# Performance work log

Measured on AMD Instinct MI355X. Metric: run time of the kernel, lower is better.

Reference implementation:

```python
import jax, jax.numpy as jnp
import numpy as np

W_CTX = 4   # sliding window half-width (self.w)
TOP = 6     # querysim top-k
KMAX = 2    # k-max pooling per n-gram


def setup_inputs() -> dict:
    key = jax.random.key(0)
    ks = jax.random.split(key, 16)
    n_words, E = 50000, 300
    B, Q, D = 128, 16, 800
    emb = jax.random.normal(ks[0], (n_words, E), jnp.float32)
    emb = emb / jnp.linalg.norm(emb, axis=1, keepdims=True)
    emb_table = jnp.concatenate([emb, jnp.zeros((1, E), jnp.float32)], 0)  # padding row
    return {
        'qrls_words': jax.random.randint(ks[1], (B, Q), 0, n_words),
        'doc_words': jax.random.randint(ks[2], (B, D), 0, n_words),
        'emb_table': emb_table,
        'idf_table': jax.random.uniform(ks[3], (n_words + 1,), jnp.float32),
        'conv1_w': jax.random.normal(ks[4], (32, 1, 1, 1), jnp.float32) * 0.1,
        'conv1_b': jnp.zeros((32,), jnp.float32),
        'conv2_w': jax.random.normal(ks[5], (32, 1, 2, 2), jnp.float32) * 0.1,
        'conv2_b': jnp.zeros((32,), jnp.float32),
        'conv3_w': jax.random.normal(ks[6], (32, 1, 3, 3), jnp.float32) * 0.1,
        'conv3_b': jnp.zeros((32,), jnp.float32),
        'w1': jax.random.normal(ks[7], (13 * Q, 32), jnp.float32) * 0.05,
        'b1': jnp.zeros((32,), jnp.float32),
        'w2': jax.random.normal(ks[8], (32, 32), jnp.float32) * 0.1,
        'b2': jnp.zeros((32,), jnp.float32),
        'w3': jax.random.normal(ks[9], (32, 1), jnp.float32) * 0.1,
        'b3': jnp.zeros((1,), jnp.float32),
    }


def _cosine_simmat(a, b):
    # a: [B,A,E], b: [B,T,E] -> [B,A,T]; denominators each get +1e-9 (as in torch code)
    an = jnp.linalg.norm(a, axis=2)[:, :, None] + 1e-9
    bn = jnp.linalg.norm(b, axis=2)[:, None, :] + 1e-9
    return jnp.einsum('bae,bte->bat', a, b) / (an * bn)


def _context(demb):
    # sliding-window sum over [max(0,i-w), min(L,i+w)) then /(2w+1)
    B, L, E = demb.shape
    csum = jnp.concatenate([jnp.zeros((B, 1, E), demb.dtype), jnp.cumsum(demb, axis=1)], axis=1)
    i = jnp.arange(L)
    s = jnp.maximum(0, i - W_CTX)
    e = jnp.minimum(L, i + W_CTX)
    return (csum[:, e] - csum[:, s]) / (2 * W_CTX + 1)


def _pacrr_conv(simmat, w, b, ng):
    # simmat: [B,1,Q,D]; pad right/bottom by ng-1, valid conv -> same Q,D
    conv = jax.lax.conv_general_dilated(
        simmat, w, (1, 1), [(0, ng - 1), (0, ng - 1)],
        dimension_numbers=('NCHW', 'OIHW', 'NCHW')) + b[None, :, None, None]
    conv = jax.nn.relu(conv)
    top_f = conv.max(axis=1)                      # max over filters: [B,Q,D]
    return jax.lax.top_k(top_f, KMAX)[0]          # k-max over doc dim: [B,Q,KMAX]


def reference(qrls_words, doc_words, emb_table, idf_table,
              conv1_w, conv1_b, conv2_w, conv2_b, conv3_w, conv3_b,
              w1, b1, w2, b2, w3, b3):
    idf = idf_table[qrls_words][..., None]                 # [B,Q,1]
    qemb = emb_table[qrls_words]                           # [B,Q,E]
    demb = emb_table[doc_words]                            # [B,D,E]
    context = _context(demb)
    querysim = jax.lax.top_k(_cosine_simmat(qemb, context), TOP)[0]  # [B,Q,TOP]
    simmat = _cosine_simmat(qemb, demb)[:, None]           # [B,1,Q,D]
    scores = jnp.concatenate([
        _pacrr_conv(simmat, conv1_w, conv1_b, 1),
        _pacrr_conv(simmat, conv2_w, conv2_b, 2),
        _pacrr_conv(simmat, conv3_w, conv3_b, 3),
    ], axis=2)                                             # [B,Q,3*KMAX]
    scores = jnp.concatenate([scores, querysim, idf], axis=-1)  # [B,Q,13]
    x = scores.reshape(scores.shape[0], -1)
    x = jax.nn.relu(x @ w1 + b1)
    x = jax.nn.relu(x @ w2 + b2)
    return x @ w3 + b3                                     # [B,1]
```

## Files before the change

### kernel.cpp

```cpp
#include <hip/hip_runtime.h>
#include <float.h>
#include <math.h>

#define NB 128
#define NQ 16
#define ND 800
#define NE 300
#define ZROW 50000

#define WS_SIM    0
#define WS_CTXINV (NB*NQ*ND)
#define WS_SCORES (WS_CTXINV + NB*ND)
#define WS_C2     (WS_SCORES + NB*NQ*13)
#define WS_QBF    (WS_C2 + NB*NQ*3*26)

#define HP 164

typedef __attribute__((ext_vector_type(8))) short short8;
typedef __attribute__((ext_vector_type(4))) float f32x4;
typedef __attribute__((ext_vector_type(4))) unsigned short ushort4v;

__device__ __forceinline__ unsigned short f2bf(float x) {
    unsigned u = __float_as_uint(x);
    u += 0x7FFF + ((u >> 16) & 1);
    return (unsigned short)(u >> 16);
}

__device__ __forceinline__ void ins6(float t[6], float v) {
    if (v > t[5]) t[5] = v;
    float a;
    if (t[5] > t[4]) { a = t[4]; t[4] = t[5]; t[5] = a; }
    if (t[4] > t[3]) { a = t[3]; t[3] = t[4]; t[4] = a; }
    if (t[3] > t[2]) { a = t[2]; t[2] = t[3]; t[3] = a; }
    if (t[2] > t[1]) { a = t[1]; t[1] = t[2]; t[2] = a; }
    if (t[1] > t[0]) { a = t[0]; t[0] = t[1]; t[1] = a; }
}

__device__ __forceinline__ void ins2(float& a1, float& a2, float v) {
    if (v > a2) a2 = v;
    if (a2 > a1) { float t = a1; a1 = a2; a2 = t; }
}

__device__ __forceinline__ void merge2(float& a1, float& a2, float b1v, float b2v) {
    float hi = fmaxf(a1, b1v), lo = fminf(a1, b1v);
    a1 = hi;
    a2 = fmaxf(lo, fmaxf(a2, b2v));
}

__global__ __launch_bounds__(256) void kq(const int* __restrict__ qrls,
                                          const float* __restrict__ emb,
                                          const float* __restrict__ idf,
                                          float* __restrict__ ws) {
    int b = blockIdx.x;
    int tid = threadIdx.x;
    __shared__ int qrow[16];
    if (tid < 16) qrow[tid] = qrls[b * NQ + tid];
    __syncthreads();
    unsigned short* qbf = (unsigned short*)(ws + WS_QBF) + (size_t)b * 16 * 320;
    for (int it = tid; it < 1200; it += 256) {
        int q = it / 75, e4 = it - q * 75;
        float4 v = *(const float4*)(emb + (size_t)qrow[q] * NE + e4 * 4);
        ushort4v u;
        u[0] = f2bf(v.x); u[1] = f2bf(v.y); u[2] = f2bf(v.z); u[3] = f2bf(v.w);
        *(ushort4v*)(qbf + q * 320 + e4 * 4) = u;
    }
    if (tid < 160) {
        int q = tid / 10, p = tid - q * 10;
        *(unsigned*)(qbf + q * 320 + 300 + p * 2) = 0u;
    }
    if (tid < NQ)
        ws[WS_SCORES + (b * NQ + tid) * 13 + 12] = idf[qrow[tid]];
}

__global__ __launch_bounds__(256, 5) void kfused(const int* __restrict__ docw,
                                                 const float* __restrict__ emb,
                                                 float* __restrict__ ws) {
    int b = blockIdx.y;
    int base = blockIdx.x * 32;
    int tid = threadIdx.x;
    __shared__ float slds[6656];
    __shared__ int sidx[40];
    __shared__ float ACC[32][33];

    int wv = tid >> 6, lane = tid & 63;

    if (tid < 40) {
        int rg = base - 4 + tid;
        sidx[tid] = (rg >= 0 && rg < ND) ? docw[b * ND + rg] : ZROW;
    }
    for (int i = tid; i < 32 * 33; i += 256) ((float*)ACC)[i] = 0.f;
    __syncthreads();

    int rsub = lane & 15, kgrp = lane >> 4;
    const unsigned short* qp = (const unsigned short*)(ws + WS_QBF)
                               + ((size_t)b * 16 + rsub) * 320 + kgrp * 8;
    int lrb = (4 + wv * 16 + rsub) * HP + kgrp * 8;
    int w0 = (wv == 3) ? 16 : 0;

    f32x4 acc = {0.f, 0.f, 0.f, 0.f};

#pragma unroll
    for (int h = 0; h < 2; ++h) {
        for (int j = wv; j < 26; j += 4) {
            int jj = __builtin_amdgcn_readfirstlane(j);
            int F = jj * 64 + lane;
            int r = F / 41;
            int c4 = F - r * 41;
            int g4 = h * 40 + c4;
            bool ok = (r < 40) && (c4 < 40) && (g4 < 75);
            int rowsrc = ok ? sidx[r] : ZROW;
            int colsrc = ok ? g4 * 4 : 0;
            const float* gp = emb + (size_t)rowsrc * NE + colsrc;
            __builtin_amdgcn_global_load_lds(
                (const __attribute__((address_space(1))) void*)gp,
                (__attribute__((address_space(3))) void*)&slds[(size_t)jj * 256],
                16, 0, 0);
        }
        __syncthreads();

        if (wv < 2) {
#pragma unroll
            for (int k = 0; k < 5; ++k) {
                int c0 = k * 32;
                float4 x0 = *(const float4*)&slds[lrb + c0];
                float4 x1 = *(const float4*)&slds[lrb + c0 + 4];
                short8 bf;
                bf[0] = (short)f2bf(x0.x); bf[1] = (short)f2bf(x0.y);
                bf[2] = (short)f2bf(x0.z); bf[3] = (short)f2bf(x0.w);
                bf[4] = (short)f2bf(x1.x); bf[5] = (short)f2bf(x1.y);
                bf[6] = (short)f2bf(x1.z); bf[7] = (short)f2bf(x1.w);
                short8 af = *(const short8*)(qp + h * 160 + c0);
                acc = __builtin_amdgcn_mfma_f32_16x16x32_bf16(af, bf, acc, 0, 0, 0);
            }
        } else {
            float cw0 = 0.f, cw1 = 0.f, cw2 = 0.f;
            for (int i = 0; i < 23; ++i) {
                int r = w0 + i;
                float2 va = *(const float2*)&slds[r * HP + 2 * lane];
                float vc = (lane < 32) ? slds[r * HP + 128 + lane] : 0.f;
                cw0 += va.x; cw1 += va.y; cw2 += vc;
                if (i >= 8) {
                    int r2 = r - 8;
                    float2 vb = *(const float2*)&slds[r2 * HP + 2 * lane];
                    float vd = (lane < 32) ? slds[r2 * HP + 128 + lane] : 0.f;
                    cw0 -= vb.x; cw1 -= vb.y; cw2 -= vd;
                }
                if (i >= 7) {
                    float s = fmaf(cw0, cw0, fmaf(cw1, cw1, cw2 * cw2));
                    s += __shfl_xor(s, 1);
                    if ((lane & 1) == 0)
                        ACC[r - 7][lane >> 1] += s;
                }
            }
        }
        __syncthreads();
    }

    if (wv < 2) {
        int col = base + wv * 16 + rsub;
        float* simp = ws + WS_SIM + (size_t)b * NQ * ND + col;
#pragma unroll
        for (int i = 0; i < 4; ++i)
            simp[(size_t)(kgrp * 4 + i) * ND] = acc[i];
    } else if (wv == 2 && lane < 32) {
        float s = 0.f;
#pragma unroll
        for (int j = 0; j < 32; ++j) s += ACC[lane][j];
        ws[WS_CTXINV + b * ND + base + lane] =
            1.f / (sqrtf(s) * (1.f / 9.f) + 1e-9f);
    }
}

__global__ __launch_bounds__(256) void ktail2(const float* __restrict__ c1w,
                                              const float* __restrict__ c1b,
                                              const float* __restrict__ c2w,
                                              const float* __restrict__ c2b,
                                              const float* __restrict__ c3w,
                                              const float* __restrict__ c3b,
                                              float* __restrict__ ws) {
    int b = blockIdx.y;
    int bx = blockIdx.x;
    int tid = threadIdx.x;
    __shared__ float BUF[3216];
    __shared__ float PART[4][16][6];
    __shared__ float WL[160 * 4];
    int wv = tid >> 6, lane = tid & 63;

    if (bx < 13) {
        if (tid < 160) {
            int f = tid / 5, j = tid - f * 5;
            float4 w;
            if (j == 0)      w = make_float4(c3w[9*f],   c3w[9*f+1], c3w[9*f+2], c3w[9*f+3]);
            else if (j == 1) w = make_float4(c3w[9*f+4], c3w[9*f+5], c3w[9*f+6], c3w[9*f+7]);
            else if (j == 2) w = make_float4(c3w[9*f+8], c3b[f],     c1w[f],     c1b[f]);
            else if (j == 3) w = make_float4(c2w[4*f],   c2w[4*f+1], c2w[4*f+2], c2w[4*f+3]);
            else             w = make_float4(c2b[f],     0.f,        0.f,        0.f);
            *(float4*)&WL[tid * 4] = w;
        }
        int c0 = bx * 64;
        for (int idx = tid; idx < 18 * 66; idx += 256) {
            int r = idx / 66, c = idx % 66;
            int d = c0 + c;
            float v = 0.f;
            if (r < NQ && d < ND) v = ws[WS_SIM + (size_t)(b * NQ + r) * ND + d];
            BUF[r * 68 + c] = v;
        }
        __syncthreads();

        int q = tid & 15, dg = tid >> 4;
        int cb = dg * 4;
        float s0[6], s1[6], s2[6];
#pragma unroll
        for (int i = 0; i < 6; ++i) {
            s0[i] = BUF[q * 68 + cb + i];
            s1[i] = BUF[(q + 1) * 68 + cb + i];
            s2[i] = BUF[(q + 2) * 68 + cb + i];
        }
        float m1[4], m2[4], m3[4];
#pragma unroll
        for (int i = 0; i < 4; ++i) { m1[i] = -FLT_MAX; m2[i] = -FLT_MAX; m3[i] = -FLT_MAX; }
        const float4* WL4 = (const float4*)WL;
        for (int f = 0; f < 32; ++f) {
            float4 wA = WL4[f * 5];
            float4 wB = WL4[f * 5 + 1];
            float4 wC = WL4[f * 5 + 2];
            float4 wD = WL4[f * 5 + 3];
            float4 wE = WL4[f * 5 + 4];
#pragma unroll
            for (int i = 0; i < 4; ++i) {
                float v1 = fmaf(wC.z, s0[i], wC.w);
                m1[i] = fmaxf(m1[i], v1);
                float v2 = wE.x;
                v2 = fmaf(wD.x, s0[i], v2); v2 = fmaf(wD.y, s0[i+1], v2);
                v2 = fmaf(wD.z, s1[i], v2); v2 = fmaf(wD.w, s1[i+1], v2);
                m2[i] = fmaxf(m2[i], v2);
                float v3 = wC.y;
                v3 = fmaf(wA.x, s0[i], v3); v3 = fmaf(wA.y, s0[i+1], v3); v3 = fmaf(wA.z, s0[i+2], v3);
                v3 = fmaf(wA.w, s1[i], v3); v3 = fmaf(wB.x, s1[i+1], v3); v3 = fmaf(wB.y, s1[i+2], v3);
                v3 = fmaf(wB.z, s2[i], v3); v3 = fmaf(wB.w, s2[i+1], v3); v3 = fmaf(wC.x, s2[i+2], v3);
                m3[i] = fmaxf(m3[i], v3);
            }
        }
        float a1[3] = {-FLT_MAX, -FLT_MAX, -FLT_MAX};
        float a2[3] = {-FLT_MAX, -FLT_MAX, -FLT_MAX};
#pragma unroll
        for (int i = 0; i < 4; ++i) {
            if (c0 + cb + i < ND) {
                ins2(a1[0], a2[0], fmaxf(m1[i], 0.f));
                ins2(a1[1], a2[1], fmaxf(m2[i], 0.f));
                ins2(a1[2], a2[2], fmaxf(m3[i], 0.f));
            }
        }
#pragma unroll
        for (int m = 16; m <= 32; m <<= 1) {
#pragma unroll
            for (int ng = 0; ng < 3; ++ng) {
                float b1v = __shfl_xor(a1[ng], m), b2v = __shfl_xor(a2[ng], m);
                merge2(a1[ng], a2[ng], b1v, b2v);
            }
        }
        if (lane < 16) {
#pragma unroll
            for (int ng = 0; ng < 3; ++ng) {
                PART[wv][lane][ng * 2]     = a1[ng];
                PART[wv][lane][ng * 2 + 1] = a2[ng];
            }
        }
        __syncthreads();
        if (tid < 16) {
            float* c2p = ws + WS_C2 + ((size_t)(b * NQ + tid) * 3) * 26 + bx * 2;
#pragma unroll
            for (int ng = 0; ng < 3; ++ng) {
                float x1 = PART[0][tid][ng * 2], x2 = PART[0][tid][ng * 2 + 1];
#pragma unroll
                for (int p = 1; p < 4; ++p)
                    merge2(x1, x2, PART[p][tid][ng * 2], PART[p][tid][ng * 2 + 1]);
                c2p[ng * 26] = x1; c2p[ng * 26 + 1] = x2;
            }
        }
    } else {
        int q = (bx - 13) * 4 + wv;
        float* P = &BUF[wv * 804];
        const float* simrow = ws + WS_SIM + (size_t)(b * NQ + q) * ND;
        const float* cinv = ws + WS_CTXINV + (size_t)b * ND;
        float carry = 0.f;
        for (int c = 0; c < 13; ++c) {
            int d = c * 64 + lane;
            float v = (d < ND) ? simrow[d] : 0.f;
#pragma unroll
            for (int off = 1; off < 64; off <<= 1) {
                float t = __shfl_up(v, off);
                if (lane >= off) v += t;
            }
            v += carry;
            if (d < ND) P[d] = v;
            carry = __shfl(v, 63);
        }
        float top[6] = {-FLT_MAX,-FLT_MAX,-FLT_MAX,-FLT_MAX,-FLT_MAX,-FLT_MAX};
        for (int c = 0; c < 13; ++c) {
            int d = c * 64 + lane;
            if (d < ND) {
                int hi_i = (d + 3 < ND) ? d + 3 : ND - 1;
                float hi = P[hi_i];
                float lo = (d >= 5) ? P[d - 5] : 0.f;
                float ctx = (hi - lo) * (1.f / 9.f) * cinv[d];
                ins6(top, ctx);
            }
        }
#pragma unroll
        for (int m = 1; m < 64; m <<= 1) {
            float o0 = __shfl_xor(top[0], m), o1 = __shfl_xor(top[1], m);
            float o2 = __shfl_xor(top[2], m), o3 = __shfl_xor(top[3], m);
            float o4 = __shfl_xor(top[4], m), o5 = __shfl_xor(top[5], m);
            ins6(top, o0); ins6(top, o1); ins6(top, o2);
            ins6(top, o3); ins6(top, o4); ins6(top, o5);
        }
        if (lane == 0) {
            float* sc = ws + WS_SCORES + (size_t)(b * NQ + q) * 13;
            sc[6] = top[0]; sc[7] = top[1]; sc[8]  = top[2];
            sc[9] = top[3]; sc[10] = top[4]; sc[11] = top[5];
        }
    }
}

__global__ __launch_bounds__(64) void kmlp(const float* __restrict__ w1,
                                           const float* __restrict__ b1,
                                           const float* __restrict__ w2,
                                           const float* __restrict__ b2,
                                           const float* __restrict__ w3,
                                           const float* __restrict__ b3,
                                           const float* __restrict__ ws,
                                           float* __restrict__ out) {
    int b = blockIdx.x, tid = threadIdx.x;
    __shared__ float sc[208];
    const float* s = ws + WS_SCORES + (size_t)b * 208;
    for (int i = tid; i < 208; i += 64)
        if ((i % 13) >= 6) sc[i] = s[i];
    if (tid < 48) {
        int q = tid / 3, ng = tid % 3;
        const float* p = ws + WS_C2 + ((size_t)(b * NQ + q) * 3 + ng) * 26;
        float x1 = p[0], x2 = p[1];
#pragma unroll
        for (int st = 1; st < 13; ++st) merge2(x1, x2, p[st * 2], p[st * 2 + 1]);
        sc[q * 13 + ng * 2] = x1; sc[q * 13 + ng * 2 + 1] = x2;
    }
    __syncthreads();
    int j = tid & 31, half = tid >> 5;
    float a = 0.f;
    int i0 = half * 104;
    for (int i = 0; i < 104; ++i) a = fmaf(sc[i0 + i], w1[(i0 + i) * 32 + j], a);
    a += __shfl_xor(a, 32);
    a = fmaxf(a + b1[j], 0.f);
    float a2v = 0.f;
    for (int k = 0; k < 32; ++k) {
        float hk = __shfl(a, k);
        a2v = fmaf(hk, w2[k * 32 + j], a2v);
    }
    a2v = fmaxf(a2v + b2[j], 0.f);
    float r = a2v * w3[j];
    if (half) r = 0.f;
#pragma unroll
    for (int m = 1; m <= 32; m <<= 1) r += __shfl_xor(r, m);
    if (tid == 0) out[b] = r + b3[0];
}

extern "C" void kernel_launch(void* const* d_in, const int* in_sizes, int n_in,
                              void* d_out, int out_size, void* d_ws, size_t ws_size,
                              hipStream_t stream) {
    (void)in_sizes; (void)n_in; (void)out_size; (void)ws_size;
    const int*   qrls = (const int*)d_in[0];
    const int*   docw = (const int*)d_in[1];
    const float* emb  = (const float*)d_in[2];
    const float* idf  = (const float*)d_in[3];
    const float* c1w  = (const float*)d_in[4];
    const float* c1b  = (const float*)d_in[5];
    const float* c2w  = (const float*)d_in[6];
    const float* c2b  = (const float*)d_in[7];
    const float* c3w  = (const float*)d_in[8];
    const float* c3b  = (const float*)d_in[9];
    const float* w1   = (const float*)d_in[10];
    const float* b1   = (const float*)d_in[11];
    const float* w2   = (const float*)d_in[12];
    const float* b2   = (const float*)d_in[13];
    const float* w3   = (const float*)d_in[14];
    const float* b3   = (const float*)d_in[15];
    float* ws  = (float*)d_ws;
    float* out = (float*)d_out;

    kq<<<dim3(NB), 256, 0, stream>>>(qrls, emb, idf, ws);
    kfused<<<dim3(25, NB), 256, 0, stream>>>(docw, emb, ws);
    ktail2<<<dim3(17, NB), 256, 0, stream>>>(c1w, c1b, c2w, c2b, c3w, c3b, ws);
    kmlp<<<dim3(NB), 64, 0, stream>>>(w1, b1, w2, b2, w3, b3, ws, out);
}
```

Before: 84.09 us.

## Double-buffer embedding staging in five column chunks to overlap loads with MFMA

The fused sim/context kernel used to stage each 160-column half of the document embeddings into LDS, then wait before computing. It now stages 64-column chunks into two alternating LDS buffers, issuing the next chunk's async global-to-LDS loads while the current chunk feeds the MFMA and sliding-window norm work. The smaller LDS footprint allows launch bounds to be raised from 5 to 6 blocks per CU, and float-to-bf16 conversion now uses the HIP intrinsic. The trade-off is more chunk iterations and barriers, and more padding loads for the final partial chunk.

```diff
diff --git a/kernel.cpp b/kernel.cpp
--- a/kernel.cpp
+++ b/kernel.cpp
@@ -1,4 +1,5 @@
 #include <hip/hip_runtime.h>
+#include <hip/hip_bf16.h>
 #include <float.h>
 #include <math.h>
 
@@ -14,16 +15,17 @@
 #define WS_C2     (WS_SCORES + NB*NQ*13)
 #define WS_QBF    (WS_C2 + NB*NQ*3*26)
 
-#define HP 164
+#define SPIT 68
+#define BUFQ 2816
 
 typedef __attribute__((ext_vector_type(8))) short short8;
 typedef __attribute__((ext_vector_type(4))) float f32x4;
 typedef __attribute__((ext_vector_type(4))) unsigned short ushort4v;
 
 __device__ __forceinline__ unsigned short f2bf(float x) {
-    unsigned u = __float_as_uint(x);
-    u += 0x7FFF + ((u >> 16) & 1);
-    return (unsigned short)(u >> 16);
+    union { __hip_bfloat16 h; unsigned short u; } cv;
+    cv.h = __float2bfloat16(x);
+    return cv.u;
 }
 
 __device__ __forceinline__ void ins6(float t[6], float v) {
@@ -72,13 +74,13 @@
         ws[WS_SCORES + (b * NQ + tid) * 13 + 12] = idf[qrow[tid]];
 }
 
-__global__ __launch_bounds__(256, 5) void kfused(const int* __restrict__ docw,
+__global__ __launch_bounds__(256, 6) void kfused(const int* __restrict__ docw,
                                                  const float* __restrict__ emb,
                                                  float* __restrict__ ws) {
     int b = blockIdx.y;
     int base = blockIdx.x * 32;
     int tid = threadIdx.x;
-    __shared__ float slds[6656];
+    __shared__ float slds[2 * BUFQ];
     __shared__ int sidx[40];
     __shared__ float ACC[32][33];
 
@@ -94,62 +96,61 @@
     int rsub = lane & 15, kgrp = lane >> 4;
     const unsigned short* qp = (const unsigned short*)(ws + WS_QBF)
                                + ((size_t)b * 16 + rsub) * 320 + kgrp * 8;
-    int lrb = (4 + wv * 16 + rsub) * HP + kgrp * 8;
+    int lrb = (4 + wv * 16 + rsub) * SPIT + kgrp * 8;
     int w0 = (wv == 3) ? 16 : 0;
 
     f32x4 acc = {0.f, 0.f, 0.f, 0.f};
 
-#pragma unroll
-    for (int h = 0; h < 2; ++h) {
-        for (int j = wv; j < 26; j += 4) {
+    auto STAGE = [&](int s, int bufsel) {
+        for (int j = wv; j < 11; j += 4) {
             int jj = __builtin_amdgcn_readfirstlane(j);
             int F = jj * 64 + lane;
-            int r = F / 41;
-            int c4 = F - r * 41;
-            int g4 = h * 40 + c4;
-            bool ok = (r < 40) && (c4 < 40) && (g4 < 75);
+            int r = F / 17;
+            int c4 = F - r * 17;
+            int g4 = s * 16 + c4;
+            bool ok = (r < 40) && (c4 < 16) && (g4 < 75);
             int rowsrc = ok ? sidx[r] : ZROW;
             int colsrc = ok ? g4 * 4 : 0;
             const float* gp = emb + (size_t)rowsrc * NE + colsrc;
             __builtin_amdgcn_global_load_lds(
                 (const __attribute__((address_space(1))) void*)gp,
-                (__attribute__((address_space(3))) void*)&slds[(size_t)jj * 256],
+                (__attribute__((address_space(3))) void*)
+                    &slds[(size_t)bufsel * BUFQ + (size_t)jj * 256],
                 16, 0, 0);
         }
-        __syncthreads();
-
+    };
+
+    STAGE(0, 0);
+    __syncthreads();
+
+    for (int s = 0; s < 5; ++s) {
+        if (s < 4) STAGE(s + 1, (s + 1) & 1);
+        int bb = (s & 1) * BUFQ;
         if (wv < 2) {
 #pragma unroll
-            for (int k = 0; k < 5; ++k) {
+            for (int k = 0; k < 2; ++k) {
                 int c0 = k * 32;
-                float4 x0 = *(const float4*)&slds[lrb + c0];
-                float4 x1 = *(const float4*)&slds[lrb + c0 + 4];
+                float4 x0 = *(const float4*)&slds[bb + lrb + c0];
+                float4 x1 = *(const float4*)&slds[bb + lrb + c0 + 4];
                 short8 bf;
                 bf[0] = (short)f2bf(x0.x); bf[1] = (short)f2bf(x0.y);
                 bf[2] = (short)f2bf(x0.z); bf[3] = (short)f2bf(x0.w);
                 bf[4] = (short)f2bf(x1.x); bf[5] = (short)f2bf(x1.y);
                 bf[6] = (short)f2bf(x1.z); bf[7] = (short)f2bf(x1.w);
-                short8 af = *(const short8*)(qp + h * 160 + c0);
+                short8 af = *(const short8*)(qp + s * 64 + c0);
                 acc = __builtin_amdgcn_mfma_f32_16x16x32_bf16(af, bf, acc, 0, 0, 0);
             }
         } else {
-            float cw0 = 0.f, cw1 = 0.f, cw2 = 0.f;
+            float cw = 0.f;
             for (int i = 0; i < 23; ++i) {
                 int r = w0 + i;
-                float2 va = *(const float2*)&slds[r * HP + 2 * lane];
-                float vc = (lane < 32) ? slds[r * HP + 128 + lane] : 0.f;
-                cw0 += va.x; cw1 += va.y; cw2 += vc;
-                if (i >= 8) {
-                    int r2 = r - 8;
-                    float2 vb = *(const float2*)&slds[r2 * HP + 2 * lane];
-                    float vd = (lane < 32) ? slds[r2 * HP + 128 + lane] : 0.f;
-                    cw0 -= vb.x; cw1 -= vb.y; cw2 -= vd;
-                }
+                cw += slds[bb + r * SPIT + lane];
+                if (i >= 8) cw -= slds[bb + (r - 8) * SPIT + lane];
                 if (i >= 7) {
-                    float s = fmaf(cw0, cw0, fmaf(cw1, cw1, cw2 * cw2));
-                    s += __shfl_xor(s, 1);
+                    float sq = cw * cw;
+                    sq += __shfl_xor(sq, 1);
                     if ((lane & 1) == 0)
-                        ACC[r - 7][lane >> 1] += s;
+                        ACC[r - 7][lane >> 1] += sq;
                 }
             }
         }
```

New measurement: 94.46 us. +12.3%, slower.

## Double-buffer embedding halves in LDS and overlap second load with first compute

Applied to the files above, without the earlier changes.

The fused similarity/context kernel now issues global-to-LDS loads for both embedding column halves up front into two separate buffers. It waits only for the first half (partial vmcnt) before computing, so the second half's load overlaps the first half's MFMA and context-norm work. It also preloads all query bf16 fragments into registers, shrinks the ACC reduction by adding one more shuffle, and switches f2bf to the HIP intrinsic. The extra LDS lowers the occupancy hint from 5 to 2 blocks per CU, which risks less latency hiding across blocks.

```diff
diff --git a/kernel.cpp b/kernel.cpp
--- a/kernel.cpp
+++ b/kernel.cpp
@@ -1,4 +1,5 @@
 #include <hip/hip_runtime.h>
+#include <hip/hip_bf16.h>
 #include <float.h>
 #include <math.h>
 
@@ -21,9 +22,9 @@
 typedef __attribute__((ext_vector_type(4))) unsigned short ushort4v;
 
 __device__ __forceinline__ unsigned short f2bf(float x) {
-    unsigned u = __float_as_uint(x);
-    u += 0x7FFF + ((u >> 16) & 1);
-    return (unsigned short)(u >> 16);
+    union { __hip_bfloat16 h; unsigned short u; } cv;
+    cv.h = __float2bfloat16(x);
+    return cv.u;
 }
 
 __device__ __forceinline__ void ins6(float t[6], float v) {
@@ -72,15 +73,16 @@
         ws[WS_SCORES + (b * NQ + tid) * 13 + 12] = idf[qrow[tid]];
 }
 
-__global__ __launch_bounds__(256, 5) void kfused(const int* __restrict__ docw,
+__global__ __launch_bounds__(256, 2) void kfused(const int* __restrict__ docw,
                                                  const float* __restrict__ emb,
                                                  float* __restrict__ ws) {
     int b = blockIdx.y;
     int base = blockIdx.x * 32;
     int tid = threadIdx.x;
-    __shared__ float slds[6656];
+    __shared__ float bufA[7168];
+    __shared__ float bufB[7168];
     __shared__ int sidx[40];
-    __shared__ float ACC[32][33];
+    __shared__ float ACC[32][17];
 
     int wv = tid >> 6, lane = tid & 63;
 
@@ -88,7 +90,7 @@
         int rg = base - 4 + tid;
         sidx[tid] = (rg >= 0 && rg < ND) ? docw[b * ND + rg] : ZROW;
     }
-    for (int i = tid; i < 32 * 33; i += 256) ((float*)ACC)[i] = 0.f;
+    for (int i = tid; i < 32 * 17; i += 256) ((float*)ACC)[i] = 0.f;
     __syncthreads();
 
     int rsub = lane & 15, kgrp = lane >> 4;
@@ -99,62 +101,121 @@
 
     f32x4 acc = {0.f, 0.f, 0.f, 0.f};
 
-#pragma unroll
-    for (int h = 0; h < 2; ++h) {
-        for (int j = wv; j < 26; j += 4) {
-            int jj = __builtin_amdgcn_readfirstlane(j);
-            int F = jj * 64 + lane;
-            int r = F / 41;
-            int c4 = F - r * 41;
-            int g4 = h * 40 + c4;
-            bool ok = (r < 40) && (c4 < 40) && (g4 < 75);
-            int rowsrc = ok ? sidx[r] : ZROW;
-            int colsrc = ok ? g4 * 4 : 0;
-            const float* gp = emb + (size_t)rowsrc * NE + colsrc;
-            __builtin_amdgcn_global_load_lds(
-                (const __attribute__((address_space(1))) void*)gp,
-                (__attribute__((address_space(3))) void*)&slds[(size_t)jj * 256],
-                16, 0, 0);
-        }
-        __syncthreads();
-
-        if (wv < 2) {
-#pragma unroll
-            for (int k = 0; k < 5; ++k) {
-                int c0 = k * 32;
-                float4 x0 = *(const float4*)&slds[lrb + c0];
-                float4 x1 = *(const float4*)&slds[lrb + c0 + 4];
-                short8 bf;
-                bf[0] = (short)f2bf(x0.x); bf[1] = (short)f2bf(x0.y);
-                bf[2] = (short)f2bf(x0.z); bf[3] = (short)f2bf(x0.w);
-                bf[4] = (short)f2bf(x1.x); bf[5] = (short)f2bf(x1.y);
-                bf[6] = (short)f2bf(x1.z); bf[7] = (short)f2bf(x1.w);
-                short8 af = *(const short8*)(qp + h * 160 + c0);
-                acc = __builtin_amdgcn_mfma_f32_16x16x32_bf16(af, bf, acc, 0, 0, 0);
-            }
-        } else {
-            float cw0 = 0.f, cw1 = 0.f, cw2 = 0.f;
-            for (int i = 0; i < 23; ++i) {
-                int r = w0 + i;
-                float2 va = *(const float2*)&slds[r * HP + 2 * lane];
-                float vc = (lane < 32) ? slds[r * HP + 128 + lane] : 0.f;
-                cw0 += va.x; cw1 += va.y; cw2 += vc;
-                if (i >= 8) {
-                    int r2 = r - 8;
-                    float2 vb = *(const float2*)&slds[r2 * HP + 2 * lane];
-                    float vd = (lane < 32) ? slds[r2 * HP + 128 + lane] : 0.f;
-                    cw0 -= vb.x; cw1 -= vb.y; cw2 -= vd;
-                }
-                if (i >= 7) {
-                    float s = fmaf(cw0, cw0, fmaf(cw1, cw1, cw2 * cw2));
-                    s += __shfl_xor(s, 1);
-                    if ((lane & 1) == 0)
-                        ACC[r - 7][lane >> 1] += s;
-                }
-            }
-        }
-        __syncthreads();
-    }
+    short8 af[10];
+    if (wv < 2) {
+#pragma unroll
+        for (int k = 0; k < 10; ++k) af[k] = *(const short8*)(qp + k * 32);
+    }
+
+#pragma unroll
+    for (int k = 0; k < 7; ++k) {
+        int jj = __builtin_amdgcn_readfirstlane(wv + k * 4);
+        int F = jj * 64 + lane;
+        int r = F / 41;
+        int c4 = F - r * 41;
+        bool ok = (r < 40) && (c4 < 40);
+        int rowsrc = ok ? sidx[(r < 40) ? r : 0] : ZROW;
+        int colsrc = ok ? c4 * 4 : 0;
+        const float* gp = emb + (size_t)rowsrc * NE + colsrc;
+        __builtin_amdgcn_global_load_lds(
+            (const __attribute__((address_space(1))) void*)gp,
+            (__attribute__((address_space(3))) void*)&bufA[(size_t)F * 4],
+            16, 0, 0);
+    }
+#pragma unroll
+    for (int k = 0; k < 7; ++k) {
+        int jj = __builtin_amdgcn_readfirstlane(wv + k * 4);
+        int F = jj * 64 + lane;
+        int r = F / 41;
+        int c4 = F - r * 41;
+        bool ok = (r < 40) && (c4 < 35);
+        int rowsrc = ok ? sidx[(r < 40) ? r : 0] : ZROW;
+        int colsrc = ok ? (160 + c4 * 4) : 0;
+        const float* gp = emb + (size_t)rowsrc * NE + colsrc;
+        __builtin_amdgcn_global_load_lds(
+            (const __attribute__((address_space(1))) void*)gp,
+            (__attribute__((address_space(3))) void*)&bufB[(size_t)F * 4],
+            16, 0, 0);
+    }
+
+    asm volatile("s_waitcnt vmcnt(7)" ::: "memory");
+    __builtin_amdgcn_sched_barrier(0);
+    __builtin_amdgcn_s_barrier();
+
+    if (wv < 2) {
+#pragma unroll
+        for (int k = 0; k < 5; ++k) {
+            int c0 = k * 32;
+            float4 x0 = *(const float4*)&bufA[lrb + c0];
+            float4 x1 = *(const float4*)&bufA[lrb + c0 + 4];
+            short8 bfv;
+            bfv[0] = (short)f2bf(x0.x); bfv[1] = (short)f2bf(x0.y);
+            bfv[2] = (short)f2bf(x0.z); bfv[3] = (short)f2bf(x0.w);
+            bfv[4] = (short)f2bf(x1.x); bfv[5] = (short)f2bf(x1.y);
+            bfv[6] = (short)f2bf(x1.z); bfv[7] = (short)f2bf(x1.w);
+            acc = __builtin_amdgcn_mfma_f32_16x16x32_bf16(af[k], bfv, acc, 0, 0, 0);
+        }
+    } else {
+        float cw0 = 0.f, cw1 = 0.f, cw2 = 0.f;
+        for (int i = 0; i < 23; ++i) {
+            int r = w0 + i;
+            float2 va = *(const float2*)&bufA[r * HP + 2 * lane];
+            float vc = (lane < 32) ? bufA[r * HP + 128 + lane] : 0.f;
+            cw0 += va.x; cw1 += va.y; cw2 += vc;
+            if (i >= 8) {
+                int r2 = r - 8;
+                float2 vb = *(const float2*)&bufA[r2 * HP + 2 * lane];
+                float vd = (lane < 32) ? bufA[r2 * HP + 128 + lane] : 0.f;
+                cw0 -= vb.x; cw1 -= vb.y; cw2 -= vd;
+            }
+            if (i >= 7) {
+                float s = fmaf(cw0, cw0, fmaf(cw1, cw1, cw2 * cw2));
+                s += __shfl_xor(s, 1);
+                s += __shfl_xor(s, 2);
+                if ((lane & 3) == 0) ACC[r - 7][lane >> 2] += s;
+            }
+        }
+    }
+
+    asm volatile("s_waitcnt vmcnt(0)" ::: "memory");
+    __builtin_amdgcn_sched_barrier(0);
+    __builtin_amdgcn_s_barrier();
+
+    if (wv < 2) {
+#pragma unroll
+        for (int k = 0; k < 5; ++k) {
+            int c0 = k * 32;
+            float4 x0 = *(const float4*)&bufB[lrb + c0];
+            float4 x1 = *(const float4*)&bufB[lrb + c0 + 4];
+            short8 bfv;
+            bfv[0] = (short)f2bf(x0.x); bfv[1] = (short)f2bf(x0.y);
+            bfv[2] = (short)f2bf(x0.z); bfv[3] = (short)f2bf(x0.w);
+            bfv[4] = (short)f2bf(x1.x); bfv[5] = (short)f2bf(x1.y);
+            bfv[6] = (short)f2bf(x1.z); bfv[7] = (short)f2bf(x1.w);
+            acc = __builtin_amdgcn_mfma_f32_16x16x32_bf16(af[5 + k], bfv, acc, 0, 0, 0);
+        }
+    } else {
+        float cw0 = 0.f, cw1 = 0.f, cw2 = 0.f;
+        for (int i = 0; i < 23; ++i) {
+            int r = w0 + i;
+            float2 va = *(const float2*)&bufB[r * HP + 2 * lane];
+            float vc = (lane < 32) ? bufB[r * HP + 128 + lane] : 0.f;
+            cw0 += va.x; cw1 += va.y; cw2 += vc;
+            if (i >= 8) {
+                int r2 = r - 8;
+                float2 vb = *(const float2*)&bufB[r2 * HP + 2 * lane];
+                float vd = (lane < 32) ? bufB[r2 * HP + 128 + lane] : 0.f;
+                cw0 -= vb.x; cw1 -= vb.y; cw2 -= vd;
+            }
+            if (i >= 7) {
+                float s = fmaf(cw0, cw0, fmaf(cw1, cw1, cw2 * cw2));
+                s += __shfl_xor(s, 1);
+                s += __shfl_xor(s, 2);
+                if ((lane & 3) == 0) ACC[r - 7][lane >> 2] += s;
+            }
+        }
+    }
+    __syncthreads();
 
     if (wv < 2) {
         int col = base + wv * 16 + rsub;
@@ -165,7 +226,7 @@
     } else if (wv == 2 && lane < 32) {
         float s = 0.f;
 #pragma unroll
-        for (int j = 0; j < 32; ++j) s += ACC[lane][j];
+        for (int j = 0; j < 16; ++j) s += ACC[lane][j];
         ws[WS_CTXINV + b * ND + base + lane] =
             1.f / (sqrtf(s) * (1.f / 9.f) + 1e-9f);
     }
```

Result: slower. 118.9 us (+41.3%).
